# Kernel tuning notes

Hardware: AMD Instinct MI355X
Metric: run time of the kernel (lower is better)

## Reference

```python
import jax, jax.numpy as jnp
import numpy as np

NEG = -1e15  # matches mask_logits constant -1000000000000000.0


def setup_inputs() -> dict:
    key = jax.random.key(0)
    ks = jax.random.split(key, 4)
    B, d, c_len, q_len = 64, 512, 1024, 128
    C = jax.random.normal(ks[0], (B, d, c_len), dtype=jnp.float32)
    Q = jax.random.normal(ks[1], (B, d, q_len), dtype=jnp.float32)
    c_mask = jnp.ones((B, c_len), dtype=jnp.float32)
    q_mask = jnp.ones((B, q_len), dtype=jnp.float32)
    W0 = jax.random.normal(ks[2], (3 * d,), dtype=jnp.float32) / np.sqrt(d).astype(np.float32)
    Wr = jax.random.normal(ks[3], (d, 4 * d), dtype=jnp.float32) * np.float32(0.02)
    return {"C": C, "Q": Q, "c_mask": c_mask, "q_mask": q_mask, "W0": W0, "Wr": Wr}


def reference(C, Q, c_mask, q_mask, W0, Wr):
    # C: [B, d, c], Q: [B, d, q]
    d = C.shape[1]
    C_t = jnp.swapaxes(C, 1, 2)  # [B, c, d]
    Q_t = jnp.swapaxes(Q, 1, 2)  # [B, q, d]
    w_c, w_q, w_m = W0[:d], W0[d:2 * d], W0[2 * d:]
    # Trilinear similarity, algebraically identical to cat([C,Q,C*Q]) @ W0
    S = (C_t @ w_c)[:, :, None] + (Q_t @ w_q)[:, None, :] \
        + jnp.einsum('bid,bjd->bij', C_t * w_m, Q_t)  # [B, c, q]
    qm = q_mask[:, None, :]  # [B, 1, q]
    cm = c_mask[:, :, None]  # [B, c, 1]
    S_bar = jax.nn.softmax(S * qm + NEG * (1.0 - qm), axis=2)
    S_bbar = jax.nn.softmax(S * cm + NEG * (1.0 - cm), axis=1)
    A = S_bar @ Q_t  # [B, c, d]
    Bm = jnp.einsum('bij,bkj->bik', S_bar, S_bbar) @ C_t  # [B, c, d]
    out = jnp.concatenate([C_t, A, C_t * A, C_t * Bm], axis=2)  # [B, c, 4d]
    # dropout inactive (eval mode); 1x1 conv == matmul with Wr [d, 4d]
    return jnp.einsum('od,bcd->boc', Wr, out)  # [B, d, c]
```

## Files before the change

kernel.cpp:

```cpp
#include <hip/hip_runtime.h>
#include <hip/hip_bf16.h>

typedef unsigned short u16;
typedef __attribute__((ext_vector_type(8))) short short8;
typedef __attribute__((ext_vector_type(4))) short short4v;
typedef __attribute__((ext_vector_type(4))) float f32x4;

#define NEGV -1000000000000000.0f
#define SBAR() asm volatile("s_barrier" ::: "memory")

__device__ __forceinline__ u16 f2bf(float f) {
  unsigned u = __float_as_uint(f);
  unsigned r = (u + 0x7FFFu + ((u >> 16) & 1u)) >> 16;
  return (u16)r;
}
__device__ __forceinline__ float bf2f(u16 s) {
  return __uint_as_float(((unsigned)s) << 16);
}
__device__ __forceinline__ void lds16(const void* g, void* l) {
  __builtin_amdgcn_global_load_lds((const __attribute__((address_space(1))) void*)g,
                                   (__attribute__((address_space(3))) void*)l,
                                   16, 0, 0);
}

__global__ __launch_bounds__(512, 2) void gemm8(const u16* __restrict__ A,
                                                const u16* __restrict__ B,
                                                float* __restrict__ out) {
  extern __shared__ u16 lds[];
  const int bid = blockIdx.x;
  const int wg = (bid & 7) * 64 + (bid >> 3);
  const int m0 = (wg & 1) * 256;
  const int n0 = (wg >> 1) * 256;
  const int tid = threadIdx.x;
  const int lane = tid & 63;
  const int w = tid >> 6;
  const int wr = w >> 2;
  const int wc = w & 3;
  const int fro = lane & 15;
  const int hi = lane >> 4;
  const int kx = fro & 7;
  const int sr = lane >> 3;
  const int sgc = ((lane & 7) ^ sr) << 3;

  const u16* Ag = A + (size_t)m0 * 2048;
  const u16* Bg = B + (size_t)n0 * 2048;

  const int rA = wr * 128 + fro;
  const int rB = wc * 64 + fro;

  f32x4 acc[8][4] = {};
  short8 aX[4][2], aY[4][2], bP[2][2], bQ[2][2];

#define STG2(gp, lp)                                                          \
  {                                                                           \
    lds16((gp) + (size_t)((w * 2 + 0) * 8 + sr) * 2048 + sgc,                 \
          (u16*)(lp) + (w * 2 + 0) * 512);                                    \
    lds16((gp) + (size_t)((w * 2 + 1) * 8 + sr) * 2048 + sgc,                 \
          (u16*)(lp) + (w * 2 + 1) * 512);                                    \
  }
#define RDF(base, row, k16) \
  (*(const short8*)&(base)[(size_t)(row) * 64 + (((k16) ^ kx) << 3)])

  STG2(Ag, lds);
  STG2(Ag + 262144, lds + 8192);
  STG2(Bg, lds + 32768);
  STG2(Bg + 262144, lds + 40960);
  STG2(Bg + 64, lds + 49152);
  STG2(Bg + 262144 + 64, lds + 57344);
  asm volatile("s_waitcnt vmcnt(4)" ::: "memory");
  SBAR();
#pragma unroll
  for (int i = 0; i < 4; ++i)
#pragma unroll
    for (int ks = 0; ks < 2; ++ks) aX[i][ks] = RDF(lds, rA + i * 16, ks * 4 + hi);

  for (int t = 0; t < 32; ++t) {
    const int cur = t & 1;
    const int nxt = cur ^ 1;
    const u16* LA = lds + cur * 16384;
    const u16* LB = lds + 32768 + cur * 16384;
    u16* LAs = lds + nxt * 16384;
    u16* LBs = lds + 32768 + cur * 16384;
    const u16* LAn = lds + nxt * 16384;
    const int kkA = (t < 31 ? t + 1 : 31) * 64;
    const int kkB = (t < 30 ? t + 2 : 31) * 64;

#pragma unroll
    for (int j = 0; j < 2; ++j)
#pragma unroll
      for (int ks = 0; ks < 2; ++ks) bP[j][ks] = RDF(LB, rB + j * 16, ks * 4 + hi);
    STG2(Ag + kkA, LAs);
    SBAR();
    __builtin_amdgcn_s_setprio(1);
#pragma unroll
    for (int i = 0; i < 4; ++i)
#pragma unroll
      for (int j = 0; j < 2; ++j)
#pragma unroll
        for (int ks = 0; ks < 2; ++ks)
          acc[i][j] = __builtin_amdgcn_mfma_f32_16x16x32_bf16(aX[i][ks], bP[j][ks],
                                                              acc[i][j], 0, 0, 0);
    __builtin_amdgcn_s_setprio(0);
    SBAR();

#pragma unroll
    for (int j = 0; j < 2; ++j)
#pragma unroll
      for (int ks = 0; ks < 2; ++ks)
        bQ[j][ks] = RDF(LB, rB + (j + 2) * 16, ks * 4 + hi);
#pragma unroll
    for (int i = 0; i < 4; ++i)
#pragma unroll
      for (int ks = 0; ks < 2; ++ks)
        aY[i][ks] = RDF(LA, rA + (i + 4) * 16, ks * 4 + hi);
    STG2(Ag + 262144 + kkA, LAs + 8192);
    SBAR();
    __builtin_amdgcn_s_setprio(1);
#pragma unroll
    for (int i = 0; i < 4; ++i)
#pragma unroll
      for (int j = 0; j < 2; ++j)
#pragma unroll
        for (int ks = 0; ks < 2; ++ks)
          acc[i][j + 2] = __builtin_amdgcn_mfma_f32_16x16x32_bf16(
              aX[i][ks], bQ[j][ks], acc[i][j + 2], 0, 0, 0);
    __builtin_amdgcn_s_setprio(0);
    SBAR();

    STG2(Bg + kkB, LBs);
    asm volatile("s_waitcnt vmcnt(2)" ::: "memory");
    SBAR();
    __builtin_amdgcn_s_setprio(1);
#pragma unroll
    for (int i = 0; i < 4; ++i)
#pragma unroll
      for (int j = 0; j < 2; ++j)
#pragma unroll
        for (int ks = 0; ks < 2; ++ks)
          acc[i + 4][j + 2] = __builtin_amdgcn_mfma_f32_16x16x32_bf16(
              aY[i][ks], bQ[j][ks], acc[i + 4][j + 2], 0, 0, 0);
    __builtin_amdgcn_s_setprio(0);
    SBAR();

#pragma unroll
    for (int i = 0; i < 4; ++i)
#pragma unroll
      for (int ks = 0; ks < 2; ++ks)
        aX[i][ks] = RDF(LAn, rA + i * 16, ks * 4 + hi);
    STG2(Bg + 262144 + kkB, LBs + 8192);
    SBAR();
    __builtin_amdgcn_s_setprio(1);
#pragma unroll
    for (int i = 0; i < 4; ++i)
#pragma unroll
      for (int j = 0; j < 2; ++j)
#pragma unroll
        for (int ks = 0; ks < 2; ++ks)
          acc[i + 4][j] = __builtin_amdgcn_mfma_f32_16x16x32_bf16(
              aY[i][ks], bP[j][ks], acc[i + 4][j], 0, 0, 0);
    __builtin_amdgcn_s_setprio(0);
    SBAR();
  }
  asm volatile("s_waitcnt vmcnt(0)" ::: "memory");

  const int crow = m0 + wr * 128 + hi * 4;
#pragma unroll
  for (int i = 0; i < 8; ++i)
#pragma unroll
    for (int j = 0; j < 4; ++j) {
      const int n = n0 + wc * 64 + j * 16 + fro;
      float* op = out + (size_t)(n >> 10) * 524288 + (n & 1023);
#pragma unroll
      for (int g = 0; g < 4; ++g)
        op[(size_t)(crow + i * 16 + g) * 1024] = acc[i][j][g];
    }
#undef STG2
#undef RDF
}

template <int EPI>
__global__ __launch_bounds__(256) void gemm_bt(
    const u16* __restrict__ A, long long sA, int lda,
    const u16* __restrict__ B, long long sB, int ldb,
    void* __restrict__ Cv, long long sC, int ldc, int K) {
  __shared__ u16 As[128 * 64];
  __shared__ u16 Bs[128 * 64];
  const int b = blockIdx.z;
  const int m0 = blockIdx.x * 128;
  const int n0 = blockIdx.y * 128;
  const u16* Ab = A + (size_t)b * sA;
  const u16* Bb = B + (size_t)b * sB;
  const int t = threadIdx.x;
  const int lane = t & 63;
  const int w = t >> 6;
  const int wr = w >> 1, wc = w & 1;
  const int srow = lane >> 3;
  const int scol = (lane & 7) * 8;

  f32x4 acc[4][4] = {};

  for (int k0 = 0; k0 < K; k0 += 64) {
    __syncthreads();
#pragma unroll
    for (int qq = 0; qq < 4; ++qq) {
      const int q = w * 4 + qq;
      const int r = q * 8 + srow;
      lds16(Ab + (size_t)(m0 + r) * lda + k0 + scol, &As[q * 512]);
      lds16(Bb + (size_t)(n0 + r) * ldb + k0 + scol, &Bs[q * 512]);
    }
    __syncthreads();
#pragma unroll
    for (int ks = 0; ks < 2; ++ks) {
      short8 af[4], bg[4];
      const int fro = lane & 15;
      const int k8 = ks * 32 + (lane >> 4) * 8;
#pragma unroll
      for (int i = 0; i < 4; ++i)
        af[i] = *(const short8*)&As[(wr * 64 + i * 16 + fro) * 64 + k8];
#pragma unroll
      for (int i = 0; i < 4; ++i)
        bg[i] = *(const short8*)&Bs[(wc * 64 + i * 16 + fro) * 64 + k8];
#pragma unroll
      for (int i = 0; i < 4; ++i)
#pragma unroll
        for (int j = 0; j < 4; ++j)
          acc[i][j] =
              __builtin_amdgcn_mfma_f32_16x16x32_bf16(af[i], bg[j], acc[i][j], 0, 0, 0);
    }
  }

  const int col = lane & 15;
  const int r4 = (lane >> 4) * 4;
#pragma unroll
  for (int i = 0; i < 4; ++i)
#pragma unroll
    for (int j = 0; j < 4; ++j) {
      const int cc = n0 + wc * 64 + j * 16 + col;
#pragma unroll
      for (int g = 0; g < 4; ++g) {
        const int rr = m0 + wr * 64 + i * 16 + r4 + g;
        if (EPI == 2)
          ((u16*)Cv)[(size_t)b * sC + (size_t)cc * ldc + rr] = f2bf(acc[i][j][g]);
      }
    }
}

__global__ __launch_bounds__(256) void gemm_s(
    const u16* __restrict__ A, const u16* __restrict__ Bq,
    const float* __restrict__ cb, const float* __restrict__ qb,
    const float* __restrict__ cmask, const float* __restrict__ qmask,
    u16* __restrict__ Sbar, u16* __restrict__ E, float* __restrict__ csum) {
  __shared__ u16 As[128 * 64];
  __shared__ u16 Bs[128 * 64];
  __shared__ float rmaxs[2][128];
  __shared__ float rsums[2][128];
  __shared__ float cparts[2][128];
  const int b = blockIdx.z;
  const int m0 = blockIdx.x * 128;
  const u16* Ab = A + (size_t)b * 2097152;
  const u16* Bb = Bq + (size_t)b * 65536;
  const int t = threadIdx.x;
  const int lane = t & 63;
  const int w = t >> 6;
  const int wr = w >> 1, wc = w & 1;
  const int srow = lane >> 3;
  const int scol = (lane & 7) * 8;

  f32x4 acc[4][4] = {};

  for (int k0 = 0; k0 < 512; k0 += 64) {
    __syncthreads();
#pragma unroll
    for (int qq = 0; qq < 4; ++qq) {
      const int q = w * 4 + qq;
      const int r = q * 8 + srow;
      lds16(Ab + (size_t)(m0 + r) * 2048 + k0 + scol, &As[q * 512]);
      lds16(Bb + (size_t)r * 512 + k0 + scol, &Bs[q * 512]);
    }
    __syncthreads();
#pragma unroll
    for (int ks = 0; ks < 2; ++ks) {
      short8 af[4], bg[4];
      const int fro = lane & 15;
      const int k8 = ks * 32 + (lane >> 4) * 8;
#pragma unroll
      for (int i = 0; i < 4; ++i)
        af[i] = *(const short8*)&As[(wr * 64 + i * 16 + fro) * 64 + k8];
#pragma unroll
      for (int i = 0; i < 4; ++i)
        bg[i] = *(const short8*)&Bs[(wc * 64 + i * 16 + fro) * 64 + k8];
#pragma unroll
      for (int i = 0; i < 4; ++i)
#pragma unroll
        for (int j = 0; j < 4; ++j)
          acc[i][j] =
              __builtin_amdgcn_mfma_f32_16x16x32_bf16(af[i], bg[j], acc[i][j], 0, 0, 0);
    }
  }

  const int fro = lane & 15;
  const int hi = lane >> 4;
  float qv[4], qbv[4];
#pragma unroll
  for (int j = 0; j < 4; ++j) {
    const int cc = wc * 64 + j * 16 + fro;
    qv[j] = qmask[b * 128 + cc];
    qbv[j] = qb[b * 128 + cc];
  }
  float colp[4] = {0.f, 0.f, 0.f, 0.f};
#pragma unroll
  for (int i = 0; i < 4; ++i)
#pragma unroll
    for (int g = 0; g < 4; ++g) {
      const int rl = wr * 64 + i * 16 + hi * 4 + g;
      const float rb = cb[b * 1024 + m0 + rl];
      const float cv = cmask[b * 1024 + m0 + rl];
      const float coff = NEGV * (1.f - cv);
#pragma unroll
      for (int j = 0; j < 4; ++j) {
        const float v = acc[i][j][g] + rb + qbv[j];
        acc[i][j][g] = v;
        const float e = __expf(v * cv + coff);
        E[((size_t)b * 1024 + m0 + rl) * 128 + wc * 64 + j * 16 + fro] = f2bf(e);
        colp[j] += e;
      }
    }
#pragma unroll
  for (int j = 0; j < 4; ++j) {
    colp[j] += __shfl_xor(colp[j], 16);
    colp[j] += __shfl_xor(colp[j], 32);
  }
  if (hi == 0)
#pragma unroll
    for (int j = 0; j < 4; ++j) cparts[wr][wc * 64 + j * 16 + fro] = colp[j];
  float rtmp[4][4];
#pragma unroll
  for (int i = 0; i < 4; ++i)
#pragma unroll
    for (int g = 0; g < 4; ++g) {
      float m = -3.4e38f;
#pragma unroll
      for (int j = 0; j < 4; ++j) {
        const float xm = acc[i][j][g] * qv[j] + NEGV * (1.f - qv[j]);
        acc[i][j][g] = xm;
        m = fmaxf(m, xm);
      }
#pragma unroll
      for (int o = 8; o; o >>= 1) m = fmaxf(m, __shfl_xor(m, o));
      rtmp[i][g] = m;
    }
  if (fro == 0)
#pragma unroll
    for (int i = 0; i < 4; ++i)
#pragma unroll
      for (int g = 0; g < 4; ++g)
        rmaxs[wc][wr * 64 + i * 16 + hi * 4 + g] = rtmp[i][g];
  __syncthreads();
  if (t < 128) atomicAdd(&csum[b * 128 + t], cparts[0][t] + cparts[1][t]);
#pragma unroll
  for (int i = 0; i < 4; ++i)
#pragma unroll
    for (int g = 0; g < 4; ++g) {
      const int rl = wr * 64 + i * 16 + hi * 4 + g;
      const float M = fmaxf(rmaxs[0][rl], rmaxs[1][rl]);
      float s = 0.f;
#pragma unroll
      for (int j = 0; j < 4; ++j) {
        const float p = __expf(acc[i][j][g] - M);
        acc[i][j][g] = p;
        s += p;
      }
#pragma unroll
      for (int o = 8; o; o >>= 1) s += __shfl_xor(s, o);
      rtmp[i][g] = s;
    }
  if (fro == 0)
#pragma unroll
    for (int i = 0; i < 4; ++i)
#pragma unroll
      for (int g = 0; g < 4; ++g)
        rsums[wc][wr * 64 + i * 16 + hi * 4 + g] = rtmp[i][g];
  __syncthreads();
#pragma unroll
  for (int i = 0; i < 4; ++i)
#pragma unroll
    for (int g = 0; g < 4; ++g) {
      const int rl = wr * 64 + i * 16 + hi * 4 + g;
      const float inv = 1.f / (rsums[0][rl] + rsums[1][rl]);
#pragma unroll
      for (int j = 0; j < 4; ++j)
        Sbar[((size_t)b * 1024 + m0 + rl) * 128 + wc * 64 + j * 16 + fro] =
            f2bf(acc[i][j][g] * inv);
    }
}

__global__ __launch_bounds__(256) void make_sbbt(const u16* __restrict__ E,
                                                 const float* __restrict__ csum,
                                                 u16* __restrict__ Sbbt) {
  __shared__ u16 L[128][130];
  __shared__ float inv[128];
  const int b = blockIdx.y;
  const int i0 = blockIdx.x * 128;
  const int t = threadIdx.x;
  if (t < 128) inv[t] = 1.f / csum[b * 128 + t];
  const int c = t & 127;
  const int r0 = t >> 7;
#pragma unroll
  for (int rr = 0; rr < 64; ++rr) {
    const int r = r0 * 64 + rr;
    L[r][c] = E[((size_t)b * 1024 + i0 + r) * 128 + c];
  }
  __syncthreads();
#pragma unroll
  for (int jj = 0; jj < 64; ++jj) {
    const int j = r0 * 64 + jj;
    Sbbt[((size_t)b * 128 + j) * 1024 + i0 + c] = f2bf(bf2f(L[c][j]) * inv[j]);
  }
}

__global__ __launch_bounds__(256) void gemm_ab(const u16* __restrict__ Sbar,
                                               const u16* __restrict__ Qo,
                                               const u16* __restrict__ Tt,
                                               u16* __restrict__ O) {
  __shared__ u16 sh[3 * 128 * 64];
  u16* As = sh;
  u16* Bq = sh + 8192;
  u16* Bt = sh + 16384;
  const int b = blockIdx.z;
  const int m0 = blockIdx.x * 128;
  const int dcol = blockIdx.y * 128;
  const u16* Ab = Sbar + (size_t)b * 131072;
  const u16* Qg = Qo + (size_t)b * 65536 + (size_t)dcol * 128;
  const u16* Tg = Tt + (size_t)b * 65536 + (size_t)dcol * 128;
  const int t = threadIdx.x;
  const int lane = t & 63;
  const int w = t >> 6;
  const int wr = w >> 1, wc = w & 1;
  const int srow = lane >> 3;
  const int scol = (lane & 7) * 8;
  const int fro = lane & 15;
  const int hi = lane >> 4;

  f32x4 aa[4][4] = {};
  f32x4 ab[4][4] = {};

  for (int k0 = 0; k0 < 128; k0 += 64) {
    __syncthreads();
#pragma unroll
    for (int qq = 0; qq < 4; ++qq) {
      const int q = w * 4 + qq;
      const int r = q * 8 + srow;
      lds16(Ab + (size_t)(m0 + r) * 128 + k0 + scol, &As[q * 512]);
      lds16(Qg + (size_t)r * 128 + k0 + scol, &Bq[q * 512]);
      lds16(Tg + (size_t)r * 128 + k0 + scol, &Bt[q * 512]);
    }
    __syncthreads();
#pragma unroll
    for (int ks = 0; ks < 2; ++ks) {
      short8 af[4], bq[4], bt[4];
      const int k8 = ks * 32 + hi * 8;
#pragma unroll
      for (int i = 0; i < 4; ++i) {
        af[i] = *(const short8*)&As[(wr * 64 + i * 16 + fro) * 64 + k8];
        bq[i] = *(const short8*)&Bq[(wc * 64 + i * 16 + fro) * 64 + k8];
        bt[i] = *(const short8*)&Bt[(wc * 64 + i * 16 + fro) * 64 + k8];
      }
#pragma unroll
      for (int i = 0; i < 4; ++i)
#pragma unroll
        for (int j = 0; j < 4; ++j) {
          aa[i][j] =
              __builtin_amdgcn_mfma_f32_16x16x32_bf16(af[i], bq[j], aa[i][j], 0, 0, 0);
          ab[i][j] =
              __builtin_amdgcn_mfma_f32_16x16x32_bf16(af[i], bt[j], ab[i][j], 0, 0, 0);
        }
    }
  }

  u16* Ls = sh;
  const int erow = t >> 4;
  const int ecol = (t & 15) * 8;
  const size_t obase0 =
      (size_t)b * 2097152 + (size_t)m0 * 2048 + dcol;
  short8 c8[8];

  __syncthreads();
#pragma unroll
  for (int i = 0; i < 4; ++i)
#pragma unroll
    for (int j = 0; j < 4; ++j)
#pragma unroll
      for (int g = 0; g < 4; ++g)
        Ls[(wr * 64 + i * 16 + hi * 4 + g) * 128 + wc * 64 + j * 16 + fro] =
            f2bf(aa[i][j][g]);
  __syncthreads();
#pragma unroll
  for (int it = 0; it < 8; ++it) {
    const int row = it * 16 + erow;
    const short8 a8 = *(const short8*)&Ls[row * 128 + ecol];
    c8[it] = *(const short8*)&O[obase0 + (size_t)row * 2048 + ecol];
    short8 p2;
#pragma unroll
    for (int k = 0; k < 8; ++k)
      p2[k] = (short)f2bf(bf2f((u16)c8[it][k]) * bf2f((u16)a8[k]));
    *(short8*)&O[obase0 + (size_t)row * 2048 + ecol + 512] = a8;
    *(short8*)&O[obase0 + (size_t)row * 2048 + ecol + 1024] = p2;
  }
  __syncthreads();
#pragma unroll
  for (int i = 0; i < 4; ++i)
#pragma unroll
    for (int j = 0; j < 4; ++j)
#pragma unroll
      for (int g = 0; g < 4; ++g)
        Ls[(wr * 64 + i * 16 + hi * 4 + g) * 128 + wc * 64 + j * 16 + fro] =
            f2bf(ab[i][j][g]);
  __syncthreads();
#pragma unroll
  for (int it = 0; it < 8; ++it) {
    const int row = it * 16 + erow;
    const short8 b8 = *(const short8*)&Ls[row * 128 + ecol];
    short8 p3;
#pragma unroll
    for (int k = 0; k < 8; ++k)
      p3[k] = (short)f2bf(bf2f((u16)c8[it][k]) * bf2f((u16)b8[k]));
    *(short8*)&O[obase0 + (size_t)row * 2048 + ecol + 1536] = p3;
  }
}

__global__ __launch_bounds__(256) void prep_C(const float* __restrict__ C,
                                              const float* __restrict__ W0,
                                              u16* __restrict__ O,
                                              u16* __restrict__ Corig,
                                              float* __restrict__ cb) {
  __shared__ float L[64][65];
  __shared__ float P[4][64];
  const int b = blockIdx.z;
  const int d0 = blockIdx.y * 64;
  const int i0 = blockIdx.x * 64;
  const int t = threadIdx.x;
  const int cx = t & 63;
  const int rb = t >> 6;
  const float* Cb = C + ((size_t)b * 512 + d0) * 1024 + i0;
  float part = 0.f;
#pragma unroll
  for (int rr = 0; rr < 16; ++rr) {
    const int r = rb * 16 + rr;
    const float v = Cb[(size_t)r * 1024 + cx];
    L[r][cx] = v;
    part = fmaf(v, W0[d0 + r], part);
    Corig[((size_t)b * 512 + d0 + r) * 1024 + i0 + cx] = f2bf(v);
  }
  P[rb][cx] = part;
  __syncthreads();
#pragma unroll
  for (int rr = 0; rr < 16; ++rr) {
    const int il = rb * 16 + rr;
    O[((size_t)b * 1024 + i0 + il) * 2048 + d0 + cx] = f2bf(L[cx][il]);
  }
  if (rb == 0)
    atomicAdd(&cb[b * 1024 + i0 + cx], P[0][cx] + P[1][cx] + P[2][cx] + P[3][cx]);
}

__global__ __launch_bounds__(256) void prep_Q(const float* __restrict__ Q,
                                              const float* __restrict__ W0,
                                              u16* __restrict__ Qmb,
                                              u16* __restrict__ Qorig,
                                              float* __restrict__ qb) {
  __shared__ float L[64][65];
  __shared__ float P[4][64];
  const int b = blockIdx.z;
  const int d0 = blockIdx.y * 64;
  const int j0 = blockIdx.x * 64;
  const int t = threadIdx.x;
  const int cx = t & 63;
  const int rb = t >> 6;
  const float* Qb = Q + ((size_t)b * 512 + d0) * 128 + j0;
  float part = 0.f;
#pragma unroll
  for (int rr = 0; rr < 16; ++rr) {
    const int r = rb * 16 + rr;
    const float v = Qb[(size_t)r * 128 + cx];
    L[r][cx] = v;
    part = fmaf(v, W0[512 + d0 + r], part);
    Qorig[((size_t)b * 512 + d0 + r) * 128 + j0 + cx] = f2bf(v);
  }
  P[rb][cx] = part;
  __syncthreads();
  const float wm = W0[1024 + d0 + cx];
#pragma unroll
  for (int rr = 0; rr < 16; ++rr) {
    const int jl = rb * 16 + rr;
    Qmb[((size_t)b * 128 + j0 + jl) * 512 + d0 + cx] = f2bf(L[cx][jl] * wm);
  }
  if (rb == 0)
    atomicAdd(&qb[b * 128 + j0 + cx], P[0][cx] + P[1][cx] + P[2][cx] + P[3][cx]);
}

__global__ __launch_bounds__(256) void cvt_wr(const float* __restrict__ Wr,
                                              u16* __restrict__ Wrb) {
  const int idx = blockIdx.x * 256 + threadIdx.x;
  const float4 v = ((const float4*)Wr)[idx];
  short4v o;
  o[0] = (short)f2bf(v.x);
  o[1] = (short)f2bf(v.y);
  o[2] = (short)f2bf(v.z);
  o[3] = (short)f2bf(v.w);
  *(short4v*)&Wrb[(size_t)idx * 4] = o;
}

extern "C" void kernel_launch(void* const* d_in, const int* in_sizes, int n_in,
                              void* d_out, int out_size, void* d_ws, size_t ws_size,
                              hipStream_t stream) {
  (void)in_sizes; (void)n_in; (void)out_size;
  const float* C = (const float*)d_in[0];
  const float* Q = (const float*)d_in[1];
  const float* cm = (const float*)d_in[2];
  const float* qm = (const float*)d_in[3];
  const float* W0 = (const float*)d_in[4];
  const float* Wr = (const float*)d_in[5];
  float* out = (float*)d_out;

  if (ws_size < 413466624ull) return;

  char* p = (char*)d_ws;
  u16* O     = (u16*)(p);
  u16* Corig = (u16*)(p + 268435456ull);
  u16* Qmb   = (u16*)(p + 335544320ull);
  u16* Qorig = (u16*)(p + 343932928ull);
  u16* E     = (u16*)(p + 352321536ull);
  u16* Sbar  = (u16*)(p + 369098752ull);
  u16* Sbbt  = (u16*)(p + 385875968ull);
  u16* Tt    = (u16*)(p + 402653184ull);
  u16* Wrb   = (u16*)(p + 411041792ull);
  float* cb  = (float*)(p + 413138944ull);
  float* qb  = (float*)(p + 413401088ull);
  float* csum= (float*)(p + 413433856ull);

  hipFuncSetAttribute((const void*)gemm8,
                      hipFuncAttributeMaxDynamicSharedMemorySize, 131072);
  hipMemsetAsync(cb, 0, 327680, stream);

  cvt_wr<<<dim3(1024), dim3(256), 0, stream>>>(Wr, Wrb);
  prep_C<<<dim3(16, 8, 64), dim3(256), 0, stream>>>(C, W0, O, Corig, cb);
  prep_Q<<<dim3(2, 8, 64), dim3(256), 0, stream>>>(Q, W0, Qmb, Qorig, qb);

  gemm_s<<<dim3(8, 1, 64), dim3(256), 0, stream>>>(O, Qmb, cb, qb, cm, qm,
                                                   Sbar, E, csum);
  make_sbbt<<<dim3(8, 64), dim3(256), 0, stream>>>(E, csum, Sbbt);

  gemm_bt<2><<<dim3(1, 4, 64), dim3(256), 0, stream>>>(
      Sbbt, 131072ll, 1024, Corig, 524288ll, 1024, Tt, 65536ll, 128, 1024);

  gemm_ab<<<dim3(8, 4, 64), dim3(256), 0, stream>>>(Sbar, Qorig, Tt, O);

  gemm8<<<dim3(512), dim3(512), 131072, stream>>>(Wrb, O, out);
}
```

Baseline: 398.5 us.

## Fuse softmax-column transpose into gemm_s and restructure final GEMM to 1024 threads

```diff
diff --git a/kernel.cpp b/kernel.cpp
--- a/kernel.cpp
+++ b/kernel.cpp
@@ -23,9 +23,9 @@
                                    16, 0, 0);
 }
 
-__global__ __launch_bounds__(512, 2) void gemm8(const u16* __restrict__ A,
-                                                const u16* __restrict__ B,
-                                                float* __restrict__ out) {
+__global__ __launch_bounds__(1024) void gemm8b(const u16* __restrict__ A,
+                                               const u16* __restrict__ B,
+                                               float* __restrict__ out) {
   extern __shared__ u16 lds[];
   const int bid = blockIdx.x;
   const int wg = (bid & 7) * 64 + (bid >> 3);
@@ -44,128 +44,79 @@
 
   const u16* Ag = A + (size_t)m0 * 2048;
   const u16* Bg = B + (size_t)n0 * 2048;
-
-  const int rA = wr * 128 + fro;
+  const int rA = wr * 64 + fro;
   const int rB = wc * 64 + fro;
 
-  f32x4 acc[8][4] = {};
-  short8 aX[4][2], aY[4][2], bP[2][2], bQ[2][2];
-
-#define STG2(gp, lp)                                                          \
-  {                                                                           \
-    lds16((gp) + (size_t)((w * 2 + 0) * 8 + sr) * 2048 + sgc,                 \
-          (u16*)(lp) + (w * 2 + 0) * 512);                                    \
-    lds16((gp) + (size_t)((w * 2 + 1) * 8 + sr) * 2048 + sgc,                 \
-          (u16*)(lp) + (w * 2 + 1) * 512);                                    \
-  }
+  f32x4 acc[4][4] = {};
+
+#define STG(gp, lp) \
+  lds16((gp) + (size_t)(w * 8 + sr) * 2048 + sgc, (u16*)(lp) + w * 512)
 #define RDF(base, row, k16) \
   (*(const short8*)&(base)[(size_t)(row) * 64 + (((k16) ^ kx) << 3)])
 
-  STG2(Ag, lds);
-  STG2(Ag + 262144, lds + 8192);
-  STG2(Bg, lds + 32768);
-  STG2(Bg + 262144, lds + 40960);
-  STG2(Bg + 64, lds + 49152);
-  STG2(Bg + 262144 + 64, lds + 57344);
-  asm volatile("s_waitcnt vmcnt(4)" ::: "memory");
+  STG(Ag, lds);
+  STG(Ag + 262144, lds + 8192);
+  STG(Bg, lds + 32768);
+  STG(Bg + 262144, lds + 32768 + 8192);
+  STG(Bg + 64, lds + 49152);
+  STG(Bg + 262144 + 64, lds + 49152 + 8192);
+  asm volatile("s_waitcnt vmcnt(2)" ::: "memory");
   SBAR();
-#pragma unroll
-  for (int i = 0; i < 4; ++i)
-#pragma unroll
-    for (int ks = 0; ks < 2; ++ks) aX[i][ks] = RDF(lds, rA + i * 16, ks * 4 + hi);
+
+  const u16* Ac = lds;
+  u16* An = lds + 16384;
+  const u16* Bc = lds + 32768;
+  const u16* Bn = lds + 49152;
+  u16* Bs2 = lds + 65536;
 
   for (int t = 0; t < 32; ++t) {
-    const int cur = t & 1;
-    const int nxt = cur ^ 1;
-    const u16* LA = lds + cur * 16384;
-    const u16* LB = lds + 32768 + cur * 16384;
-    u16* LAs = lds + nxt * 16384;
-    u16* LBs = lds + 32768 + cur * 16384;
-    const u16* LAn = lds + nxt * 16384;
     const int kkA = (t < 31 ? t + 1 : 31) * 64;
     const int kkB = (t < 30 ? t + 2 : 31) * 64;
-
-#pragma unroll
-    for (int j = 0; j < 2; ++j)
-#pragma unroll
-      for (int ks = 0; ks < 2; ++ks) bP[j][ks] = RDF(LB, rB + j * 16, ks * 4 + hi);
-    STG2(Ag + kkA, LAs);
+    short8 af[4], bf[4];
+
+#pragma unroll
+    for (int i = 0; i < 4; ++i) af[i] = RDF(Ac, rA + i * 16, hi);
+#pragma unroll
+    for (int j = 0; j < 4; ++j) bf[j] = RDF(Bc, rB + j * 16, hi);
+    STG(Ag + kkA, An);
+    STG(Ag + 262144 + kkA, An + 8192);
     SBAR();
     __builtin_amdgcn_s_setprio(1);
 #pragma unroll
     for (int i = 0; i < 4; ++i)
 #pragma unroll
-      for (int j = 0; j < 2; ++j)
-#pragma unroll
-        for (int ks = 0; ks < 2; ++ks)
-          acc[i][j] = __builtin_amdgcn_mfma_f32_16x16x32_bf16(aX[i][ks], bP[j][ks],
-                                                              acc[i][j], 0, 0, 0);
+      for (int j = 0; j < 4; ++j)
+        acc[i][j] =
+            __builtin_amdgcn_mfma_f32_16x16x32_bf16(af[i], bf[j], acc[i][j], 0, 0, 0);
     __builtin_amdgcn_s_setprio(0);
     SBAR();
 
 #pragma unroll
-    for (int j = 0; j < 2; ++j)
-#pragma unroll
-      for (int ks = 0; ks < 2; ++ks)
-        bQ[j][ks] = RDF(LB, rB + (j + 2) * 16, ks * 4 + hi);
-#pragma unroll
-    for (int i = 0; i < 4; ++i)
-#pragma unroll
-      for (int ks = 0; ks < 2; ++ks)
-        aY[i][ks] = RDF(LA, rA + (i + 4) * 16, ks * 4 + hi);
-    STG2(Ag + 262144 + kkA, LAs + 8192);
-    SBAR();
-    __builtin_amdgcn_s_setprio(1);
-#pragma unroll
-    for (int i = 0; i < 4; ++i)
-#pragma unroll
-      for (int j = 0; j < 2; ++j)
-#pragma unroll
-        for (int ks = 0; ks < 2; ++ks)
-          acc[i][j + 2] = __builtin_amdgcn_mfma_f32_16x16x32_bf16(
-              aX[i][ks], bQ[j][ks], acc[i][j + 2], 0, 0, 0);
-    __builtin_amdgcn_s_setprio(0);
-    SBAR();
-
-    STG2(Bg + kkB, LBs);
+    for (int i = 0; i < 4; ++i) af[i] = RDF(Ac, rA + i * 16, 4 + hi);
+#pragma unroll
+    for (int j = 0; j < 4; ++j) bf[j] = RDF(Bc, rB + j * 16, 4 + hi);
+    STG(Bg + kkB, Bs2);
+    STG(Bg + 262144 + kkB, Bs2 + 8192);
     asm volatile("s_waitcnt vmcnt(2)" ::: "memory");
     SBAR();
     __builtin_amdgcn_s_setprio(1);
 #pragma unroll
     for (int i = 0; i < 4; ++i)
 #pragma unroll
-      for (int j = 0; j < 2; ++j)
-#pragma unroll
-        for (int ks = 0; ks < 2; ++ks)
-          acc[i + 4][j + 2] = __builtin_amdgcn_mfma_f32_16x16x32_bf16(
-              aY[i][ks], bQ[j][ks], acc[i + 4][j + 2], 0, 0, 0);
+      for (int j = 0; j < 4; ++j)
+        acc[i][j] =
+            __builtin_amdgcn_mfma_f32_16x16x32_bf16(af[i], bf[j], acc[i][j], 0, 0, 0);
     __builtin_amdgcn_s_setprio(0);
     SBAR();
 
-#pragma unroll
-    for (int i = 0; i < 4; ++i)
-#pragma unroll
-      for (int ks = 0; ks < 2; ++ks)
-        aX[i][ks] = RDF(LAn, rA + i * 16, ks * 4 + hi);
-    STG2(Bg + 262144 + kkB, LBs + 8192);
-    SBAR();
-    __builtin_amdgcn_s_setprio(1);
-#pragma unroll
-    for (int i = 0; i < 4; ++i)
-#pragma unroll
-      for (int j = 0; j < 2; ++j)
-#pragma unroll
-        for (int ks = 0; ks < 2; ++ks)
-          acc[i + 4][j] = __builtin_amdgcn_mfma_f32_16x16x32_bf16(
-              aY[i][ks], bP[j][ks], acc[i + 4][j], 0, 0, 0);
-    __builtin_amdgcn_s_setprio(0);
-    SBAR();
+    u16* tA = An; An = (u16*)Ac; Ac = tA;
+    u16* tB = (u16*)Bc; Bc = Bn; Bn = Bs2; Bs2 = tB;
   }
   asm volatile("s_waitcnt vmcnt(0)" ::: "memory");
 
-  const int crow = m0 + wr * 128 + hi * 4;
-#pragma unroll
-  for (int i = 0; i < 8; ++i)
+  const int crow = m0 + wr * 64 + hi * 4;
+#pragma unroll
+  for (int i = 0; i < 4; ++i)
 #pragma unroll
     for (int j = 0; j < 4; ++j) {
       const int n = n0 + wc * 64 + j * 16 + fro;
@@ -174,22 +125,20 @@
       for (int g = 0; g < 4; ++g)
         op[(size_t)(crow + i * 16 + g) * 1024] = acc[i][j][g];
     }
-#undef STG2
+#undef STG
 #undef RDF
 }
 
-template <int EPI>
-__global__ __launch_bounds__(256) void gemm_bt(
-    const u16* __restrict__ A, long long sA, int lda,
-    const u16* __restrict__ B, long long sB, int ldb,
-    void* __restrict__ Cv, long long sC, int ldc, int K) {
+__global__ __launch_bounds__(256) void gemm_t(const u16* __restrict__ A,
+                                              const u16* __restrict__ B,
+                                              const float* __restrict__ csum,
+                                              u16* __restrict__ Tt) {
   __shared__ u16 As[128 * 64];
   __shared__ u16 Bs[128 * 64];
   const int b = blockIdx.z;
-  const int m0 = blockIdx.x * 128;
   const int n0 = blockIdx.y * 128;
-  const u16* Ab = A + (size_t)b * sA;
-  const u16* Bb = B + (size_t)b * sB;
+  const u16* Ab = A + (size_t)b * 131072;
+  const u16* Bb = B + (size_t)b * 524288;
   const int t = threadIdx.x;
   const int lane = t & 63;
   const int w = t >> 6;
@@ -199,14 +148,14 @@
 
   f32x4 acc[4][4] = {};
 
-  for (int k0 = 0; k0 < K; k0 += 64) {
+  for (int k0 = 0; k0 < 1024; k0 += 64) {
     __syncthreads();
 #pragma unroll
     for (int qq = 0; qq < 4; ++qq) {
       const int q = w * 4 + qq;
       const int r = q * 8 + srow;
-      lds16(Ab + (size_t)(m0 + r) * lda + k0 + scol, &As[q * 512]);
-      lds16(Bb + (size_t)(n0 + r) * ldb + k0 + scol, &Bs[q * 512]);
+      lds16(Ab + (size_t)r * 1024 + k0 + scol, &As[q * 512]);
+      lds16(Bb + (size_t)(n0 + r) * 1024 + k0 + scol, &Bs[q * 512]);
     }
     __syncthreads();
 #pragma unroll
@@ -234,13 +183,13 @@
 #pragma unroll
   for (int i = 0; i < 4; ++i)
 #pragma unroll
-    for (int j = 0; j < 4; ++j) {
-      const int cc = n0 + wc * 64 + j * 16 + col;
-#pragma unroll
-      for (int g = 0; g < 4; ++g) {
-        const int rr = m0 + wr * 64 + i * 16 + r4 + g;
-        if (EPI == 2)
-          ((u16*)Cv)[(size_t)b * sC + (size_t)cc * ldc + rr] = f2bf(acc[i][j][g]);
+    for (int g = 0; g < 4; ++g) {
+      const int rr = wr * 64 + i * 16 + r4 + g;
+      const float inv = 1.f / csum[b * 128 + rr];
+#pragma unroll
+      for (int j = 0; j < 4; ++j) {
+        const int cc = n0 + wc * 64 + j * 16 + col;
+        Tt[(size_t)b * 65536 + (size_t)cc * 128 + rr] = f2bf(acc[i][j][g] * inv);
       }
     }
 }
@@ -249,9 +198,10 @@
     const u16* __restrict__ A, const u16* __restrict__ Bq,
     const float* __restrict__ cb, const float* __restrict__ qb,
     const float* __restrict__ cmask, const float* __restrict__ qmask,
-    u16* __restrict__ Sbar, u16* __restrict__ E, float* __restrict__ csum) {
+    u16* __restrict__ Sbar, u16* __restrict__ EunT, float* __restrict__ csum) {
   __shared__ u16 As[128 * 64];
   __shared__ u16 Bs[128 * 64];
+  __shared__ u16 Lt[128][136];
   __shared__ float rmaxs[2][128];
   __shared__ float rsums[2][128];
   __shared__ float cparts[2][128];
@@ -321,7 +271,7 @@
         const float v = acc[i][j][g] + rb + qbv[j];
         acc[i][j][g] = v;
         const float e = __expf(v * cv + coff);
-        E[((size_t)b * 1024 + m0 + rl) * 128 + wc * 64 + j * 16 + fro] = f2bf(e);
+        Lt[wc * 64 + j * 16 + fro][rl] = f2bf(e);
         colp[j] += e;
       }
     }
@@ -357,6 +307,14 @@
         rmaxs[wc][wr * 64 + i * 16 + hi * 4 + g] = rtmp[i][g];
   __syncthreads();
   if (t < 128) atomicAdd(&csum[b * 128 + t], cparts[0][t] + cparts[1][t]);
+  {
+    const int jr = t >> 1;
+    const int ih = (t & 1) * 64;
+    u16* dst = EunT + (size_t)b * 131072 + (size_t)jr * 1024 + m0 + ih;
+#pragma unroll
+    for (int s = 0; s < 8; ++s)
+      *(short8*)(dst + s * 8) = *(const short8*)&Lt[jr][ih + s * 8];
+  }
 #pragma unroll
   for (int i = 0; i < 4; ++i)
 #pragma unroll
@@ -392,30 +350,6 @@
         Sbar[((size_t)b * 1024 + m0 + rl) * 128 + wc * 64 + j * 16 + fro] =
             f2bf(acc[i][j][g] * inv);
     }
-}
-
-__global__ __launch_bounds__(256) void make_sbbt(const u16* __restrict__ E,
-                                                 const float* __restrict__ csum,
-                                                 u16* __restrict__ Sbbt) {
-  __shared__ u16 L[128][130];
-  __shared__ float inv[128];
-  const int b = blockIdx.y;
-  const int i0 = blockIdx.x * 128;
-  const int t = threadIdx.x;
-  if (t < 128) inv[t] = 1.f / csum[b * 128 + t];
-  const int c = t & 127;
-  const int r0 = t >> 7;
-#pragma unroll
-  for (int rr = 0; rr < 64; ++rr) {
-    const int r = r0 * 64 + rr;
-    L[r][c] = E[((size_t)b * 1024 + i0 + r) * 128 + c];
-  }
-  __syncthreads();
-#pragma unroll
-  for (int jj = 0; jj < 64; ++jj) {
-    const int j = r0 * 64 + jj;
-    Sbbt[((size_t)b * 128 + j) * 1024 + i0 + c] = f2bf(bf2f(L[c][j]) * inv[j]);
-  }
 }
 
 __global__ __launch_bounds__(256) void gemm_ab(const u16* __restrict__ Sbar,
@@ -480,8 +414,7 @@
   u16* Ls = sh;
   const int erow = t >> 4;
   const int ecol = (t & 15) * 8;
-  const size_t obase0 =
-      (size_t)b * 2097152 + (size_t)m0 * 2048 + dcol;
+  const size_t obase0 = (size_t)b * 2097152 + (size_t)m0 * 2048 + dcol;
   short8 c8[8];
 
   __syncthreads();
@@ -621,24 +554,23 @@
   const float* Wr = (const float*)d_in[5];
   float* out = (float*)d_out;
 
-  if (ws_size < 413466624ull) return;
+  if (ws_size < 405078016ull) return;
 
   char* p = (char*)d_ws;
   u16* O     = (u16*)(p);
   u16* Corig = (u16*)(p + 268435456ull);
   u16* Qmb   = (u16*)(p + 335544320ull);
   u16* Qorig = (u16*)(p + 343932928ull);
-  u16* E     = (u16*)(p + 352321536ull);
-  u16* Sbar  = (u16*)(p + 369098752ull);
-  u16* Sbbt  = (u16*)(p + 385875968ull);
-  u16* Tt    = (u16*)(p + 402653184ull);
-  u16* Wrb   = (u16*)(p + 411041792ull);
-  float* cb  = (float*)(p + 413138944ull);
-  float* qb  = (float*)(p + 413401088ull);
-  float* csum= (float*)(p + 413433856ull);
-
-  hipFuncSetAttribute((const void*)gemm8,
-                      hipFuncAttributeMaxDynamicSharedMemorySize, 131072);
+  u16* EunT  = (u16*)(p + 360710144ull);
+  u16* Sbar  = (u16*)(p + 377487360ull);
+  u16* Tt    = (u16*)(p + 394264576ull);
+  u16* Wrb   = (u16*)(p + 402653184ull);
+  float* cb  = (float*)(p + 404750336ull);
+  float* qb  = (float*)(p + 405012480ull);
+  float* csum= (float*)(p + 405045248ull);
+
+  hipFuncSetAttribute((const void*)gemm8b,
+                      hipFuncAttributeMaxDynamicSharedMemorySize, 163840);
   hipMemsetAsync(cb, 0, 327680, stream);
 
   cvt_wr<<<dim3(1024), dim3(256), 0, stream>>>(Wr, Wrb);
@@ -646,13 +578,11 @@
   prep_Q<<<dim3(2, 8, 64), dim3(256), 0, stream>>>(Q, W0, Qmb, Qorig, qb);
 
   gemm_s<<<dim3(8, 1, 64), dim3(256), 0, stream>>>(O, Qmb, cb, qb, cm, qm,
-                                                   Sbar, E, csum);
-  make_sbbt<<<dim3(8, 64), dim3(256), 0, stream>>>(E, csum, Sbbt);
-
-  gemm_bt<2><<<dim3(1, 4, 64), dim3(256), 0, stream>>>(
-      Sbbt, 131072ll, 1024, Corig, 524288ll, 1024, Tt, 65536ll, 128, 1024);
+                                                   Sbar, EunT, csum);
+
+  gemm_t<<<dim3(1, 4, 64), dim3(256), 0, stream>>>(EunT, Corig, csum, Tt);
 
   gemm_ab<<<dim3(8, 4, 64), dim3(256), 0, stream>>>(Sbar, Qorig, Tt, O);
 
-  gemm8<<<dim3(512), dim3(512), 131072, stream>>>(Wrb, O, out);
-}
+  gemm8b<<<dim3(512), dim3(1024), 163840, stream>>>(Wrb, O, out);
+}
```

Measured after the change: 368.4 us. -7.6%, faster.
